# Performance work log

Measured on AMD Instinct MI355X. Metric: run time of the kernel, lower is better.

The kernel has to match this reference:

```python
import jax, jax.numpy as jnp
import numpy as np

N = 100000
E = 1600000
IN_DIM, HID_DIM, OUT_DIM = 128, 64, 32
HEADS = 8
NEG_SLOPE = 0.2
NEG_INF = -1e9


def _glorot(key, shape):
    stdv = np.sqrt(6.0 / (shape[-2] + shape[-1]))
    return jax.random.uniform(key, shape, jnp.float32, -stdv, stdv)


def gat_conv(x, src, dst, self_mask, W, att, bias, heads, out_ch, concat):
    """One GATConv layer (eval mode: dropout off). src/dst already include self-loops;
    self_mask marks original edges that were self-loops (removed via -inf score)."""
    n = x.shape[0]
    h = (x @ W).reshape(n, heads, out_ch)              # [N,H,C]
    x_i = h[dst]                                        # [Etot,H,C] gather target
    x_j = h[src]                                        # [Etot,H,C] gather source
    a = jnp.einsum('ehc,hc->eh', x_i, att[0, :, :out_ch]) \
        + jnp.einsum('ehc,hc->eh', x_j, att[0, :, out_ch:])
    alpha = jax.nn.leaky_relu(a, NEG_SLOPE)             # [Etot,H]
    alpha = jnp.where(self_mask[:, None], NEG_INF, alpha)
    amax = jax.lax.stop_gradient(
        jax.ops.segment_max(alpha, dst, num_segments=n))
    ex = jnp.exp(alpha - amax[dst])
    denom = jax.ops.segment_sum(ex, dst, num_segments=n)
    w = ex / denom[dst]                                 # segment softmax over incoming edges
    out = jax.ops.segment_sum(x_j * w[:, :, None], dst, num_segments=n)  # [N,H,C]
    out = out.reshape(n, heads * out_ch) if concat else out.mean(axis=1)
    return out + bias


def setup_inputs() -> dict:
    key = jax.random.key(0)
    ks = jax.random.split(key, 12)
    x = jax.random.normal(ks[0], (N, IN_DIM), jnp.float32)
    edge_index = jax.random.randint(ks[1], (2, E), 0, N, jnp.int64)
    c1 = HID_DIM // HEADS  # 8
    params = {
        'W1': _glorot(ks[2], (IN_DIM, HEADS * c1)),
        'att1': _glorot(ks[3], (1, HEADS, 2 * c1)),
        'b1': jnp.zeros((HID_DIM,), jnp.float32),
        'W2': _glorot(ks[4], (HID_DIM, HEADS * c1)),
        'att2': _glorot(ks[5], (1, HEADS, 2 * c1)),
        'b2': jnp.zeros((HID_DIM,), jnp.float32),
        'W3': _glorot(ks[6], (HID_DIM, 1 * OUT_DIM)),
        'att3': _glorot(ks[7], (1, 1, 2 * OUT_DIM)),
        'b3': jnp.zeros((OUT_DIM,), jnp.float32),
    }
    return dict(x=x, edge_index=edge_index, **params)


def reference(x, edge_index, W1, att1, b1, W2, att2, b2, W3, att3, b3):
    n = x.shape[0]
    src, dst = edge_index[0], edge_index[1]
    loop = jnp.arange(n, dtype=src.dtype)
    src_f = jnp.concatenate([src, loop])
    dst_f = jnp.concatenate([dst, loop])
    # remove_self_loops + add_self_loops: mask original self-loops, append fresh ones
    self_mask = jnp.concatenate([src == dst, jnp.zeros((n,), bool)])
    c1 = HID_DIM // HEADS
    h = jax.nn.elu(gat_conv(x, src_f, dst_f, self_mask, W1, att1, b1, HEADS, c1, True))
    h = jax.nn.elu(gat_conv(h, src_f, dst_f, self_mask, W2, att2, b2, HEADS, c1, True))
    out = gat_conv(h, src_f, dst_f, self_mask, W3, att3, b3, 1, OUT_DIM, False)
    return out
```

## Files before the change

kernel.cpp:

```cpp
#include <hip/hip_runtime.h>
#include <hip/hip_bf16.h>

#define NN 100000
#define EE 1600000

constexpr int SCAN_BLK = 1024;
constexpr int NB_SCAN  = (NN + SCAN_BLK - 1) / SCAN_BLK;

constexpr int NR2 = 8;
constexpr int RSZ = NN / NR2;
constexpr int CH  = 32;
constexpr int CSZ = EE / CH;
constexpr int SCAT_B = CH * NR2;


__global__ __launch_bounds__(256) void histL_k(const int* __restrict__ ei,
                                               int* __restrict__ CntG) {
    __shared__ int cnt[RSZ];
    int r = blockIdx.x % NR2, c = blockIdx.x / NR2;
    int lo = r * RSZ;
    for (int t = threadIdx.x; t < RSZ; t += 256) cnt[t] = 0;
    __syncthreads();
    const int* __restrict__ dstp = ei + EE;
    int base = c * CSZ;
    int tid = threadIdx.x;
    for (int ii = 0; ii < CSZ; ii += 1024) {
        int off = ii + tid * 4;
        if (off < CSZ) {
            int4 s4 = *(const int4*)&ei[base + off];
            int4 d4 = *(const int4*)&dstp[base + off];
            int dl;
            dl = d4.x - lo; if (dl >= 0 && dl < RSZ && s4.x != d4.x) atomicAdd(&cnt[dl], 1);
            dl = d4.y - lo; if (dl >= 0 && dl < RSZ && s4.y != d4.y) atomicAdd(&cnt[dl], 1);
            dl = d4.z - lo; if (dl >= 0 && dl < RSZ && s4.z != d4.z) atomicAdd(&cnt[dl], 1);
            dl = d4.w - lo; if (dl >= 0 && dl < RSZ && s4.w != d4.w) atomicAdd(&cnt[dl], 1);
        }
    }
    __syncthreads();
    for (int t = threadIdx.x; t < RSZ; t += 256)
        CntG[(size_t)c * NN + lo + t] = cnt[t];
}

__global__ __launch_bounds__(256) void combine_sum_k(int* __restrict__ CntG,
                                                     int* __restrict__ deg,
                                                     int* __restrict__ partials) {
    __shared__ int sh[256];
    int t = threadIdx.x;
    int s_tot = 0;
    #pragma unroll
    for (int k = 0; k < 4; ++k) {
        int d = blockIdx.x * SCAN_BLK + k * 256 + t;
        int run = 0;
        if (d < NN) {
            #pragma unroll 8
            for (int c = 0; c < CH; ++c) {
                int v = CntG[(size_t)c * NN + d];
                CntG[(size_t)c * NN + d] = run;
                run += v;
            }
            deg[d] = run;
        }
        s_tot += run;
    }
    sh[t] = s_tot; __syncthreads();
    for (int off = 128; off > 0; off >>= 1) {
        if (t < off) sh[t] += sh[t + off];
        __syncthreads();
    }
    if (t == 0) partials[blockIdx.x] = sh[0];
}

__global__ void scan_final(const int* __restrict__ deg, const int* __restrict__ partials,
                           int* __restrict__ rowptr) {
    __shared__ int sh[256];
    __shared__ int sp[128];
    int t = threadIdx.x;
    if (t < 128) sp[t] = (t < NB_SCAN) ? partials[t] : 0;
    __syncthreads();
    for (int off = 1; off < 128; off <<= 1) {
        int tmp = 0;
        if (t < 128 && t >= off) tmp = sp[t - off];
        __syncthreads();
        if (t < 128) sp[t] += tmp;
        __syncthreads();
    }
    int pref0 = sp[blockIdx.x] - partials[blockIdx.x];

    int base = blockIdx.x * SCAN_BLK + t * 4;
    int v[4]; int s = 0;
    #pragma unroll
    for (int k = 0; k < 4; ++k) { int i = base + k; v[k] = (i < NN) ? deg[i] : 0; s += v[k]; }
    sh[t] = s; __syncthreads();
    for (int off = 1; off < 256; off <<= 1) {
        int tmp = (t >= off) ? sh[t - off] : 0;
        __syncthreads();
        sh[t] += tmp;
        __syncthreads();
    }
    int pref = pref0 + sh[t] - s;
    #pragma unroll
    for (int k = 0; k < 4; ++k) {
        int i = base + k;
        if (i < NN) {
            rowptr[i] = pref; pref += v[k];
            if (i == NN - 1) rowptr[NN] = pref;
        }
    }
}


__global__ __launch_bounds__(256) void sg1_k(const int* __restrict__ ei,
                                             const int* __restrict__ CntG,
                                             const int* __restrict__ rowptr,
                                             int* __restrict__ col,
                                             const float* __restrict__ xin,
                                             const float* __restrict__ W,
                                             const float* __restrict__ att,
                                             uint2* __restrict__ Hbf,
                                             float* __restrict__ ssrcA,
                                             float* __restrict__ sdst) {
    extern __shared__ char smem[];
    int tid = threadIdx.x;

    if (blockIdx.x < SCAT_B) {
        int* cur = (int*)smem;
        int r = blockIdx.x % NR2, c = blockIdx.x / NR2;
        int lo = r * RSZ;
        for (int t = tid; t < RSZ; t += 256)
            cur[t] = rowptr[lo + t] + CntG[(size_t)c * NN + lo + t];
        __syncthreads();
        const int* __restrict__ dstp = ei + EE;
        int base = c * CSZ;
        for (int ii = 0; ii < CSZ; ii += 1024) {
            int off = ii + tid * 4;
            if (off < CSZ) {
                int4 s4 = *(const int4*)&ei[base + off];
                int4 d4 = *(const int4*)&dstp[base + off];
                int dl;
                dl = d4.x - lo; if (dl >= 0 && dl < RSZ && s4.x != d4.x) { int p = atomicAdd(&cur[dl], 1); col[p] = s4.x; }
                dl = d4.y - lo; if (dl >= 0 && dl < RSZ && s4.y != d4.y) { int p = atomicAdd(&cur[dl], 1); col[p] = s4.y; }
                dl = d4.z - lo; if (dl >= 0 && dl < RSZ && s4.z != d4.z) { int p = atomicAdd(&cur[dl], 1); col[p] = s4.z; }
                dl = d4.w - lo; if (dl >= 0 && dl < RSZ && s4.w != d4.w) { int p = atomicAdd(&cur[dl], 1); col[p] = s4.w; }
            }
        }
        return;
    }

    constexpr int K = 128, M = 64, Hh = 8, NPB = 64;
    constexpr int C   = M / Hh;
    constexpr int MG  = M / 4;
    constexpr int K4  = K / 4;
    constexpr int KC4 = 16;
    constexpr int NCH = K4 / KC4;

    float4* Wq = (float4*)smem;
    float4* Xq = Wq + K * MG;

    const float4* W4 = (const float4*)W;
    for (int i = tid; i < K * MG; i += 256) Wq[i] = W4[i];

    int node0 = (blockIdx.x - SCAT_B) * NPB;
    const float4* x4 = (const float4*)xin;

    int mg = tid % MG, ng = tid / MG;
    int nb = ng * 4;
    float acc[4][4];
    #pragma unroll
    for (int i = 0; i < 4; ++i)
        #pragma unroll
        for (int j = 0; j < 4; ++j) acc[i][j] = 0.f;

    for (int ch = 0; ch < NCH; ++ch) {
        __syncthreads();
        for (int i = tid; i < NPB * KC4; i += 256) {
            int n = i / KC4, k4l = i % KC4;
            int node = node0 + n;
            float4 v = make_float4(0.f, 0.f, 0.f, 0.f);
            if (node < NN) v = x4[(size_t)node * K4 + ch * KC4 + k4l];
            Xq[i] = v;
        }
        __syncthreads();
        #pragma unroll 4
        for (int k4 = 0; k4 < KC4; ++k4) {
            float4 xv[4], wv[4];
            #pragma unroll
            for (int i = 0; i < 4; ++i) xv[i] = Xq[(nb + i) * KC4 + k4];
            int kbase = (ch * KC4 + k4) * 4;
            #pragma unroll
            for (int kk = 0; kk < 4; ++kk) wv[kk] = Wq[(kbase + kk) * MG + mg];
            #pragma unroll
            for (int i = 0; i < 4; ++i) {
                const float* xf = (const float*)&xv[i];
                #pragma unroll
                for (int kk = 0; kk < 4; ++kk) {
                    const float* wf = (const float*)&wv[kk];
                    float xs = xf[kk];
                    acc[i][0] = fmaf(xs, wf[0], acc[i][0]);
                    acc[i][1] = fmaf(xs, wf[1], acc[i][1]);
                    acc[i][2] = fmaf(xs, wf[2], acc[i][2]);
                    acc[i][3] = fmaf(xs, wf[3], acc[i][3]);
                }
            }
        }
    }

    constexpr int TPH = C / 4;
    int head = mg / TPH;
    int c0   = (mg % TPH) * 4;
    float ad[4], as_[4];
    #pragma unroll
    for (int j = 0; j < 4; ++j) {
        ad[j]  = att[head * 2 * C + c0 + j];
        as_[j] = att[head * 2 * C + C + c0 + j];
    }
    #pragma unroll
    for (int i = 0; i < 4; ++i) {
        int node = node0 + nb + i;
        if (node < NN) {
            unsigned short us[4];
            #pragma unroll
            for (int j = 0; j < 4; ++j) {
                __hip_bfloat16 b = __float2bfloat16(acc[i][j]);
                us[j] = *(unsigned short*)&b;
            }
            uint2 pk;
            pk.x = (unsigned)us[0] | ((unsigned)us[1] << 16);
            pk.y = (unsigned)us[2] | ((unsigned)us[3] << 16);
            Hbf[(size_t)node * MG + mg] = pk;
        }
        float pd = acc[i][0]*ad[0]  + acc[i][1]*ad[1]  + acc[i][2]*ad[2]  + acc[i][3]*ad[3];
        float ps = acc[i][0]*as_[0] + acc[i][1]*as_[1] + acc[i][2]*as_[2] + acc[i][3]*as_[3];
        #pragma unroll
        for (int off = 1; off < TPH; off <<= 1) {
            pd += __shfl_xor(pd, off, 64);
            ps += __shfl_xor(ps, off, 64);
        }
        if ((mg % TPH) == 0 && node < NN) {
            sdst[node * Hh + head]  = pd;
            ssrcA[node * Hh + head] = ps;
        }
    }
}


template<int K, int M, int H, int NPB>
__global__ __launch_bounds__(256) void gemm_tile(const float* __restrict__ xin,
                          const float* __restrict__ W,
                          const float* __restrict__ att,
                          uint2* __restrict__ Hbf,
                          float* __restrict__ ssrcA,
                          float* __restrict__ sdst) {
    constexpr int C   = M / H;
    constexpr int MG  = M / 4;
    constexpr int NG  = NPB / 4;
    static_assert(MG * NG == 256, "tile mismatch");
    constexpr int K4  = K / 4;
    constexpr int KC4 = (K4 > 16) ? 16 : K4;
    constexpr int NCH = K4 / KC4;

    __shared__ float4 Wq[K * MG];
    __shared__ float4 Xq[NPB * KC4];

    int tid = threadIdx.x;
    const float4* W4 = (const float4*)W;
    for (int i = tid; i < K * MG; i += 256) Wq[i] = W4[i];

    int node0 = blockIdx.x * NPB;
    const float4* x4 = (const float4*)xin;

    int mg = tid % MG, ng = tid / MG;
    int nb = ng * 4;
    float acc[4][4];
    #pragma unroll
    for (int i = 0; i < 4; ++i)
        #pragma unroll
        for (int j = 0; j < 4; ++j) acc[i][j] = 0.f;

    for (int ch = 0; ch < NCH; ++ch) {
        __syncthreads();
        for (int i = tid; i < NPB * KC4; i += 256) {
            int n = i / KC4, k4l = i % KC4;
            int node = node0 + n;
            float4 v = make_float4(0.f, 0.f, 0.f, 0.f);
            if (node < NN) v = x4[(size_t)node * K4 + ch * KC4 + k4l];
            Xq[i] = v;
        }
        __syncthreads();
        #pragma unroll 4
        for (int k4 = 0; k4 < KC4; ++k4) {
            float4 xv[4], wv[4];
            #pragma unroll
            for (int i = 0; i < 4; ++i) xv[i] = Xq[(nb + i) * KC4 + k4];
            int kbase = (ch * KC4 + k4) * 4;
            #pragma unroll
            for (int kk = 0; kk < 4; ++kk) wv[kk] = Wq[(kbase + kk) * MG + mg];
            #pragma unroll
            for (int i = 0; i < 4; ++i) {
                const float* xf = (const float*)&xv[i];
                #pragma unroll
                for (int kk = 0; kk < 4; ++kk) {
                    const float* wf = (const float*)&wv[kk];
                    float xs = xf[kk];
                    acc[i][0] = fmaf(xs, wf[0], acc[i][0]);
                    acc[i][1] = fmaf(xs, wf[1], acc[i][1]);
                    acc[i][2] = fmaf(xs, wf[2], acc[i][2]);
                    acc[i][3] = fmaf(xs, wf[3], acc[i][3]);
                }
            }
        }
    }

    constexpr int TPH = C / 4;
    int head = mg / TPH;
    int c0   = (mg % TPH) * 4;
    float ad[4], as_[4];
    #pragma unroll
    for (int j = 0; j < 4; ++j) {
        ad[j]  = att[head * 2 * C + c0 + j];
        as_[j] = att[head * 2 * C + C + c0 + j];
    }
    #pragma unroll
    for (int i = 0; i < 4; ++i) {
        int node = node0 + nb + i;
        if (node < NN) {
            unsigned short us[4];
            #pragma unroll
            for (int j = 0; j < 4; ++j) {
                __hip_bfloat16 b = __float2bfloat16(acc[i][j]);
                us[j] = *(unsigned short*)&b;
            }
            uint2 pk;
            pk.x = (unsigned)us[0] | ((unsigned)us[1] << 16);
            pk.y = (unsigned)us[2] | ((unsigned)us[3] << 16);
            Hbf[(size_t)node * MG + mg] = pk;
        }
        float pd = acc[i][0]*ad[0]  + acc[i][1]*ad[1]  + acc[i][2]*ad[2]  + acc[i][3]*ad[3];
        float ps = acc[i][0]*as_[0] + acc[i][1]*as_[1] + acc[i][2]*as_[2] + acc[i][3]*as_[3];
        #pragma unroll
        for (int off = 1; off < TPH; off <<= 1) {
            pd += __shfl_xor(pd, off, 64);
            ps += __shfl_xor(ps, off, 64);
        }
        if ((mg % TPH) == 0 && node < NN) {
            sdst[node * H + head]  = pd;
            ssrcA[node * H + head] = ps;
        }
    }
}


template<int CT, int H, int U, bool ELU_OUT>
__global__ __launch_bounds__(256) void agg_k(const int* __restrict__ rowptr, const int* __restrict__ col,
                      const float* __restrict__ sdst, const float* __restrict__ ssrcA,
                      const uint2* __restrict__ Hbf,
                      const float* __restrict__ bias, float* __restrict__ output) {
    constexpr int C    = CT / H;
    constexpr int CP   = CT / 4;
    constexpr int G    = 64 / CP;
    constexpr int NL   = U / G;
    constexpr int EPEL = (U * H >= 64) ? (U * H) / 64 : 1;
    static_assert(EPEL == 1 || EPEL == 2, "mapping");

    int lane = threadIdx.x & 63;
    int node = blockIdx.x * (blockDim.x >> 6) + (threadIdx.x >> 6);
    if (node >= NN) return;

    int cp = lane % CP;
    int pp = lane / CP;
    int hh = (4 * cp) / C;
    int eh = lane % H;
    int gb = lane / H;
    bool elane = (lane < U * H);

    float sd = elane ? sdst[node * H + eh] : 0.f;

    int start = rowptr[node], end = rowptr[node + 1];

    float dsum = 0.f;
    float e_self = 0.f;
    if (lane < H) {
        float ss = ssrcA[node * H + lane];
        float a = sd + ss; a = (a >= 0.f) ? a : 0.2f * a;
        e_self = __expf(a);
        dsum = e_self;
    }
    uint2 hs = Hbf[(size_t)node * CP + cp];
    float exs = __shfl(e_self, hh, 64);
    float4 acc = make_float4(0.f, 0.f, 0.f, 0.f);
    if (pp == 0) {
        acc.x = exs * __uint_as_float(hs.x << 16);
        acc.y = exs * __uint_as_float(hs.x & 0xffff0000u);
        acc.z = exs * __uint_as_float(hs.y << 16);
        acc.w = exs * __uint_as_float(hs.y & 0xffff0000u);
    }

    int cv = node;
    if (start < end) {
        int idx = start + lane;
        if (lane < U && idx < end) cv = col[idx];
    }

    for (int j = start; j < end; j += U) {
        float s1 = 0.f, s2 = 0.f;
        int b1 = 0, b2 = 0;
        if (EPEL == 2) {
            b1 = __shfl(cv, gb, 64);
            b2 = __shfl(cv, gb + U / 2, 64);
            s1 = ssrcA[b1 * H + eh];
            s2 = ssrcA[b2 * H + eh];
        } else {
            b1 = __shfl(cv, gb, 64);
            if (elane) s1 = ssrcA[b1 * H + eh];
        }

        uint2 hv[NL];
        #pragma unroll
        for (int t = 0; t < NL; ++t) {
            int se = __shfl(cv, t * G + pp, 64);
            hv[t] = Hbf[(size_t)se * CP + cp];
        }

        int jn = j + U;
        int cvN = node;
        if (jn < end) {
            int idx = jn + lane;
            if (lane < U && idx < end) cvN = col[idx];
        }

        float e1 = 0.f, e2 = 0.f;
        if (EPEL == 2) {
            float a1 = sd + s1; a1 = (a1 >= 0.f) ? a1 : 0.2f * a1;
            float a2 = sd + s2; a2 = (a2 >= 0.f) ? a2 : 0.2f * a2;
            if (j + gb < end)         e1 = __expf(a1);
            if (j + gb + U / 2 < end) e2 = __expf(a2);
            dsum += e1 + e2;
        } else {
            float a1 = sd + s1; a1 = (a1 >= 0.f) ? a1 : 0.2f * a1;
            if (elane && j + gb < end) { e1 = __expf(a1); dsum += e1; }
        }

        #pragma unroll
        for (int t = 0; t < NL; ++t) {
            int eidx = t * G + pp;
            float ex;
            if (EPEL == 2)
                ex = __shfl((t * G + G - 1 < U / 2) ? e1 : e2, (eidx & (U / 2 - 1)) * H + hh, 64);
            else
                ex = __shfl(e1, eidx * H + hh, 64);
            float f0 = __uint_as_float(hv[t].x << 16);
            float f1 = __uint_as_float(hv[t].x & 0xffff0000u);
            float f2 = __uint_as_float(hv[t].y << 16);
            float f3 = __uint_as_float(hv[t].y & 0xffff0000u);
            acc.x = fmaf(ex, f0, acc.x);
            acc.y = fmaf(ex, f1, acc.y);
            acc.z = fmaf(ex, f2, acc.z);
            acc.w = fmaf(ex, f3, acc.w);
        }
        cv = cvN;
    }

    #pragma unroll
    for (int off = H; off < 64; off <<= 1) dsum += __shfl_xor(dsum, off, 64);
    float den = __shfl(dsum, hh, 64);
    #pragma unroll
    for (int off = CP; off < 64; off <<= 1) {
        acc.x += __shfl_xor(acc.x, off, 64);
        acc.y += __shfl_xor(acc.y, off, 64);
        acc.z += __shfl_xor(acc.z, off, 64);
        acc.w += __shfl_xor(acc.w, off, 64);
    }
    if (lane < CP) {
        float inv = 1.f / den;
        float4 bv = ((const float4*)bias)[cp];
        float4 v;
        v.x = acc.x * inv + bv.x;
        v.y = acc.y * inv + bv.y;
        v.z = acc.z * inv + bv.z;
        v.w = acc.w * inv + bv.w;
        if (ELU_OUT) {
            v.x = (v.x > 0.f) ? v.x : expm1f(v.x);
            v.y = (v.y > 0.f) ? v.y : expm1f(v.y);
            v.z = (v.z > 0.f) ? v.z : expm1f(v.z);
            v.w = (v.w > 0.f) ? v.w : expm1f(v.w);
        }
        ((float4*)output)[(size_t)node * CP + cp] = v;
    }
}


extern "C" void kernel_launch(void* const* d_in, const int* in_sizes, int n_in,
                              void* d_out, int out_size, void* d_ws, size_t ws_size,
                              hipStream_t stream) {
    const float* x    = (const float*)d_in[0];
    const int*   ei   = (const int*)d_in[1];
    const float* W1   = (const float*)d_in[2];
    const float* att1 = (const float*)d_in[3];
    const float* b1   = (const float*)d_in[4];
    const float* W2   = (const float*)d_in[5];
    const float* att2 = (const float*)d_in[6];
    const float* b2   = (const float*)d_in[7];
    const float* W3   = (const float*)d_in[8];
    const float* att3 = (const float*)d_in[9];
    const float* b3   = (const float*)d_in[10];
    float* out = (float*)d_out;

    char* p = (char*)d_ws;
    auto alloc = [&](size_t bytes) -> void* {
        void* r = (void*)p;
        p += (bytes + 255) & ~(size_t)255;
        return r;
    };
    int*   rowptr   = (int*)alloc((NN + 1) * sizeof(int));
    int*   deg      = (int*)alloc(NN * sizeof(int));
    int*   CntG     = (int*)alloc((size_t)CH * NN * sizeof(int));
    int*   partials = (int*)alloc(NB_SCAN * sizeof(int));
    int*   col      = (int*)alloc(EE * sizeof(int));
    float* sdst     = (float*)alloc((size_t)NN * 8 * sizeof(float));
    float* ssrcA    = (float*)alloc((size_t)NN * 8 * sizeof(float));
    uint2* Hbf      = (uint2*)alloc((size_t)NN * 16 * sizeof(uint2));
    float* Fb       = (float*)alloc((size_t)NN * 64 * sizeof(float));

    histL_k<<<CH * NR2, 256, 0, stream>>>(ei, CntG);
    combine_sum_k<<<NB_SCAN, 256, 0, stream>>>(CntG, deg, partials);
    scan_final<<<NB_SCAN, 256, 0, stream>>>(deg, partials, rowptr);

    constexpr int SMEM = RSZ * (int)sizeof(int);
    sg1_k<<<SCAT_B + (NN + 63) / 64, 256, SMEM, stream>>>(ei, CntG, rowptr, col,
                                                          x, W1, att1, Hbf, ssrcA, sdst);

    agg_k<64, 8, 16, true><<<(NN + 3) / 4, 256, 0, stream>>>(rowptr, col, sdst, ssrcA, Hbf, b1, Fb);

    gemm_tile<64, 64, 8, 64><<<(NN + 63) / 64, 256, 0, stream>>>(Fb, W2, att2, Hbf, ssrcA, sdst);
    agg_k<64, 8, 16, true><<<(NN + 3) / 4, 256, 0, stream>>>(rowptr, col, sdst, ssrcA, Hbf, b2, Fb);

    gemm_tile<64, 32, 1, 128><<<(NN + 127) / 128, 256, 0, stream>>>(Fb, W3, att3, Hbf, ssrcA, sdst);
    agg_k<32, 1, 32, false><<<(NN + 3) / 4, 256, 0, stream>>>(rowptr, col, sdst, ssrcA, Hbf, b3, out);
}
```

Baseline: 385.5 us.

## Fuse layer aggregation and GEMM stages into one cooperative persistent kernel

Replaces the five per-layer launches (three aggregations, two GEMMs) with one cooperative persistent kernel. Phases are separated by grid-wide syncs, and each block loops over node tiles in grid-stride fashion. Buffers are split per layer, with Hbf2 aliased onto the scratch count buffer, and the GEMM K-chunk is reduced to 8 so the shared memory fits a single union. The aim is to remove launch gaps and tail effects between stages. The cost is grid.sync overhead, an occupancy limit of 5 blocks per CU that caps parallelism, and worse latency hiding in the gather-heavy aggregation phases.

```diff
diff --git a/kernel.cpp b/kernel.cpp
--- a/kernel.cpp
+++ b/kernel.cpp
@@ -1,5 +1,8 @@
 #include <hip/hip_runtime.h>
 #include <hip/hip_bf16.h>
+#include <hip/hip_cooperative_groups.h>
+
+namespace cg = cooperative_groups;
 
 #define NN 100000
 #define EE 1600000
@@ -243,72 +246,171 @@
 }
 
 
-template<int K, int M, int H, int NPB>
-__global__ __launch_bounds__(256) void gemm_tile(const float* __restrict__ xin,
-                          const float* __restrict__ W,
-                          const float* __restrict__ att,
-                          uint2* __restrict__ Hbf,
-                          float* __restrict__ ssrcA,
-                          float* __restrict__ sdst) {
+template<int CT, int H, int U, bool ELU_OUT>
+__device__ void agg_phase(const int* __restrict__ rowptr, const int* __restrict__ col,
+                          const float* __restrict__ sdst, const float* __restrict__ ssrcA,
+                          const uint2* __restrict__ Hbf,
+                          const float* __restrict__ bias, float* __restrict__ output) {
+    constexpr int C    = CT / H;
+    constexpr int CP   = CT / 4;
+    constexpr int G    = 64 / CP;
+    constexpr int NL   = U / G;
+    constexpr int EPEL = (U * H >= 64) ? (U * H) / 64 : 1;
+    static_assert(EPEL == 1 || EPEL == 2, "mapping");
+    constexpr int NU   = (NN + 3) / 4;
+
+    int lane = threadIdx.x & 63;
+    int wid  = threadIdx.x >> 6;
+    int cp = lane % CP;
+    int pp = lane / CP;
+    int hh = (4 * cp) / C;
+    int eh = lane % H;
+    int gb = lane / H;
+    bool elane = (lane < U * H);
+
+    for (int u = blockIdx.x; u < NU; u += gridDim.x) {
+        int node = u * 4 + wid;
+        if (node >= NN) continue;
+
+        float sd = elane ? sdst[node * H + eh] : 0.f;
+        int start = rowptr[node], end = rowptr[node + 1];
+
+        float dsum = 0.f;
+        float e_self = 0.f;
+        if (lane < H) {
+            float ss = ssrcA[node * H + lane];
+            float a = sd + ss; a = (a >= 0.f) ? a : 0.2f * a;
+            e_self = __expf(a);
+            dsum = e_self;
+        }
+        uint2 hs = Hbf[(size_t)node * CP + cp];
+        float exs = __shfl(e_self, hh, 64);
+        float4 acc = make_float4(0.f, 0.f, 0.f, 0.f);
+        if (pp == 0) {
+            acc.x = exs * __uint_as_float(hs.x << 16);
+            acc.y = exs * __uint_as_float(hs.x & 0xffff0000u);
+            acc.z = exs * __uint_as_float(hs.y << 16);
+            acc.w = exs * __uint_as_float(hs.y & 0xffff0000u);
+        }
+
+        int cv = node;
+        if (start < end) {
+            int idx = start + lane;
+            if (lane < U && idx < end) cv = col[idx];
+        }
+
+        for (int j = start; j < end; j += U) {
+            float s1 = 0.f, s2 = 0.f;
+            int b1 = 0, b2 = 0;
+            if (EPEL == 2) {
+                b1 = __shfl(cv, gb, 64);
+                b2 = __shfl(cv, gb + U / 2, 64);
+                s1 = ssrcA[b1 * H + eh];
+                s2 = ssrcA[b2 * H + eh];
+            } else {
+                b1 = __shfl(cv, gb, 64);
+                if (elane) s1 = ssrcA[b1 * H + eh];
+            }
+
+            uint2 hv[NL];
+            #pragma unroll
+            for (int t = 0; t < NL; ++t) {
+                int se = __shfl(cv, t * G + pp, 64);
+                hv[t] = Hbf[(size_t)se * CP + cp];
+            }
+
+            int jn = j + U;
+            int cvN = node;
+            if (jn < end) {
+                int idx = jn + lane;
+                if (lane < U && idx < end) cvN = col[idx];
+            }
+
+            float e1 = 0.f, e2 = 0.f;
+            if (EPEL == 2) {
+                float a1 = sd + s1; a1 = (a1 >= 0.f) ? a1 : 0.2f * a1;
+                float a2 = sd + s2; a2 = (a2 >= 0.f) ? a2 : 0.2f * a2;
+                if (j + gb < end)         e1 = __expf(a1);
+                if (j + gb + U / 2 < end) e2 = __expf(a2);
+                dsum += e1 + e2;
+            } else {
+                float a1 = sd + s1; a1 = (a1 >= 0.f) ? a1 : 0.2f * a1;
+                if (elane && j + gb < end) { e1 = __expf(a1); dsum += e1; }
+            }
+
+            #pragma unroll
+            for (int t = 0; t < NL; ++t) {
+                int eidx = t * G + pp;
+                float ex;
+                if (EPEL == 2)
+                    ex = __shfl((t * G + G - 1 < U / 2) ? e1 : e2, (eidx & (U / 2 - 1)) * H + hh, 64);
+                else
+                    ex = __shfl(e1, eidx * H + hh, 64);
+                float f0 = __uint_as_float(hv[t].x << 16);
+                float f1 = __uint_as_float(hv[t].x & 0xffff0000u);
+                float f2 = __uint_as_float(hv[t].y << 16);
+                float f3 = __uint_as_float(hv[t].y & 0xffff0000u);
+                acc.x = fmaf(ex, f0, acc.x);
+                acc.y = fmaf(ex, f1, acc.y);
+                acc.z = fmaf(ex, f2, acc.z);
+                acc.w = fmaf(ex, f3, acc.w);
+            }
+            cv = cvN;
+        }
+
+        #pragma unroll
+        for (int off = H; off < 64; off <<= 1) dsum += __shfl_xor(dsum, off, 64);
+        float den = __shfl(dsum, hh, 64);
+        #pragma unroll
+        for (int off = CP; off < 64; off <<= 1) {
+            acc.x += __shfl_xor(acc.x, off, 64);
+            acc.y += __shfl_xor(acc.y, off, 64);
+            acc.z += __shfl_xor(acc.z, off, 64);
+            acc.w += __shfl_xor(acc.w, off, 64);
+        }
+        if (lane < CP) {
+            float inv = 1.f / den;
+            float4 bv = ((const float4*)bias)[cp];
+            float4 v;
+            v.x = acc.x * inv + bv.x;
+            v.y = acc.y * inv + bv.y;
+            v.z = acc.z * inv + bv.z;
+            v.w = acc.w * inv + bv.w;
+            if (ELU_OUT) {
+                v.x = (v.x > 0.f) ? v.x : expm1f(v.x);
+                v.y = (v.y > 0.f) ? v.y : expm1f(v.y);
+                v.z = (v.z > 0.f) ? v.z : expm1f(v.z);
+                v.w = (v.w > 0.f) ? v.w : expm1f(v.w);
+            }
+            ((float4*)output)[(size_t)node * CP + cp] = v;
+        }
+    }
+}
+
+
+template<int K, int M, int H, int NPB, int KC4>
+__device__ void gemm_phase(const float* __restrict__ xin,
+                           const float* __restrict__ W,
+                           const float* __restrict__ att,
+                           uint2* __restrict__ Hbf,
+                           float* __restrict__ ssrcA,
+                           float* __restrict__ sdst,
+                           float4* __restrict__ Wq, float4* __restrict__ Xq) {
     constexpr int C   = M / H;
     constexpr int MG  = M / 4;
     constexpr int NG  = NPB / 4;
     static_assert(MG * NG == 256, "tile mismatch");
     constexpr int K4  = K / 4;
-    constexpr int KC4 = (K4 > 16) ? 16 : K4;
     constexpr int NCH = K4 / KC4;
-
-    __shared__ float4 Wq[K * MG];
-    __shared__ float4 Xq[NPB * KC4];
+    constexpr int NT  = (NN + NPB - 1) / NPB;
 
     int tid = threadIdx.x;
     const float4* W4 = (const float4*)W;
     for (int i = tid; i < K * MG; i += 256) Wq[i] = W4[i];
 
-    int node0 = blockIdx.x * NPB;
     const float4* x4 = (const float4*)xin;
-
     int mg = tid % MG, ng = tid / MG;
     int nb = ng * 4;
-    float acc[4][4];
-    #pragma unroll
-    for (int i = 0; i < 4; ++i)
-        #pragma unroll
-        for (int j = 0; j < 4; ++j) acc[i][j] = 0.f;
-
-    for (int ch = 0; ch < NCH; ++ch) {
-        __syncthreads();
-        for (int i = tid; i < NPB * KC4; i += 256) {
-            int n = i / KC4, k4l = i % KC4;
-            int node = node0 + n;
-            float4 v = make_float4(0.f, 0.f, 0.f, 0.f);
-            if (node < NN) v = x4[(size_t)node * K4 + ch * KC4 + k4l];
-            Xq[i] = v;
-        }
-        __syncthreads();
-        #pragma unroll 4
-        for (int k4 = 0; k4 < KC4; ++k4) {
-            float4 xv[4], wv[4];
-            #pragma unroll
-            for (int i = 0; i < 4; ++i) xv[i] = Xq[(nb + i) * KC4 + k4];
-            int kbase = (ch * KC4 + k4) * 4;
-            #pragma unroll
-            for (int kk = 0; kk < 4; ++kk) wv[kk] = Wq[(kbase + kk) * MG + mg];
-            #pragma unroll
-            for (int i = 0; i < 4; ++i) {
-                const float* xf = (const float*)&xv[i];
-                #pragma unroll
-                for (int kk = 0; kk < 4; ++kk) {
-                    const float* wf = (const float*)&wv[kk];
-                    float xs = xf[kk];
-                    acc[i][0] = fmaf(xs, wf[0], acc[i][0]);
-                    acc[i][1] = fmaf(xs, wf[1], acc[i][1]);
-                    acc[i][2] = fmaf(xs, wf[2], acc[i][2]);
-                    acc[i][3] = fmaf(xs, wf[3], acc[i][3]);
-                }
-            }
-        }
-    }
 
     constexpr int TPH = C / 4;
     int head = mg / TPH;
@@ -319,172 +421,127 @@
         ad[j]  = att[head * 2 * C + c0 + j];
         as_[j] = att[head * 2 * C + C + c0 + j];
     }
-    #pragma unroll
-    for (int i = 0; i < 4; ++i) {
-        int node = node0 + nb + i;
-        if (node < NN) {
-            unsigned short us[4];
-            #pragma unroll
-            for (int j = 0; j < 4; ++j) {
-                __hip_bfloat16 b = __float2bfloat16(acc[i][j]);
-                us[j] = *(unsigned short*)&b;
-            }
-            uint2 pk;
-            pk.x = (unsigned)us[0] | ((unsigned)us[1] << 16);
-            pk.y = (unsigned)us[2] | ((unsigned)us[3] << 16);
-            Hbf[(size_t)node * MG + mg] = pk;
-        }
-        float pd = acc[i][0]*ad[0]  + acc[i][1]*ad[1]  + acc[i][2]*ad[2]  + acc[i][3]*ad[3];
-        float ps = acc[i][0]*as_[0] + acc[i][1]*as_[1] + acc[i][2]*as_[2] + acc[i][3]*as_[3];
+
+    for (int u = blockIdx.x; u < NT; u += gridDim.x) {
+        int node0 = u * NPB;
+        float acc[4][4];
         #pragma unroll
-        for (int off = 1; off < TPH; off <<= 1) {
-            pd += __shfl_xor(pd, off, 64);
-            ps += __shfl_xor(ps, off, 64);
-        }
-        if ((mg % TPH) == 0 && node < NN) {
-            sdst[node * H + head]  = pd;
-            ssrcA[node * H + head] = ps;
-        }
-    }
+        for (int i = 0; i < 4; ++i)
+            #pragma unroll
+            for (int j = 0; j < 4; ++j) acc[i][j] = 0.f;
+
+        for (int ch = 0; ch < NCH; ++ch) {
+            __syncthreads();
+            for (int i = tid; i < NPB * KC4; i += 256) {
+                int n = i / KC4, k4l = i % KC4;
+                int node = node0 + n;
+                float4 v = make_float4(0.f, 0.f, 0.f, 0.f);
+                if (node < NN) v = x4[(size_t)node * K4 + ch * KC4 + k4l];
+                Xq[i] = v;
+            }
+            __syncthreads();
+            #pragma unroll 4
+            for (int k4 = 0; k4 < KC4; ++k4) {
+                float4 xv[4], wv[4];
+                #pragma unroll
+                for (int i = 0; i < 4; ++i) xv[i] = Xq[(nb + i) * KC4 + k4];
+                int kbase = (ch * KC4 + k4) * 4;
+                #pragma unroll
+                for (int kk = 0; kk < 4; ++kk) wv[kk] = Wq[(kbase + kk) * MG + mg];
+                #pragma unroll
+                for (int i = 0; i < 4; ++i) {
+                    const float* xf = (const float*)&xv[i];
+                    #pragma unroll
+                    for (int kk = 0; kk < 4; ++kk) {
+                        const float* wf = (const float*)&wv[kk];
+                        float xs = xf[kk];
+                        acc[i][0] = fmaf(xs, wf[0], acc[i][0]);
+                        acc[i][1] = fmaf(xs, wf[1], acc[i][1]);
+                        acc[i][2] = fmaf(xs, wf[2], acc[i][2]);
+                        acc[i][3] = fmaf(xs, wf[3], acc[i][3]);
+                    }
+                }
+            }
+        }
+
+        #pragma unroll
+        for (int i = 0; i < 4; ++i) {
+            int node = node0 + nb + i;
+            if (node < NN) {
+                unsigned short us[4];
+                #pragma unroll
+                for (int j = 0; j < 4; ++j) {
+                    __hip_bfloat16 b = __float2bfloat16(acc[i][j]);
+                    us[j] = *(unsigned short*)&b;
+                }
+                uint2 pk;
+                pk.x = (unsigned)us[0] | ((unsigned)us[1] << 16);
+                pk.y = (unsigned)us[2] | ((unsigned)us[3] << 16);
+                Hbf[(size_t)node * MG + mg] = pk;
+            }
+            float pd = acc[i][0]*ad[0]  + acc[i][1]*ad[1]  + acc[i][2]*ad[2]  + acc[i][3]*ad[3];
+            float ps = acc[i][0]*as_[0] + acc[i][1]*as_[1] + acc[i][2]*as_[2] + acc[i][3]*as_[3];
+            #pragma unroll
+            for (int off = 1; off < TPH; off <<= 1) {
+                pd += __shfl_xor(pd, off, 64);
+                ps += __shfl_xor(ps, off, 64);
+            }
+            if ((mg % TPH) == 0 && node < NN) {
+                sdst[node * H + head]  = pd;
+                ssrcA[node * H + head] = ps;
+            }
+        }
+    }
+}
+
+
+__global__ __launch_bounds__(256, 5) void layers_k(
+    const int* rowptr, const int* col,
+    const float* sdst1, const float* ssrcA1, const uint2* Hbf1, const float* b1,
+    float* Fb,
+    const float* W2, const float* att2, uint2* Hbf2, float* ssrcA2, float* sdst2,
+    const float* b2,
+    const float* W3, const float* att3, uint2* Hbf3, float* ssrcA3, float* sdst3,
+    const float* b3,
+    float* out)
+{
+    __shared__ float4 smemU[1536];
+    cg::grid_group grid = cg::this_grid();
+
+    agg_phase<64, 8, 16, true>(rowptr, col, sdst1, ssrcA1, Hbf1, b1, Fb);
+    __threadfence(); grid.sync(); __threadfence();
+
+    gemm_phase<64, 64, 8, 64, 8>(Fb, W2, att2, Hbf2, ssrcA2, sdst2,
+                                 smemU, smemU + 1024);
+    __threadfence(); grid.sync(); __threadfence();
+
+    agg_phase<64, 8, 16, true>(rowptr, col, sdst2, ssrcA2, Hbf2, b2, Fb);
+    __threadfence(); grid.sync(); __threadfence();
+
+    gemm_phase<64, 32, 1, 128, 8>(Fb, W3, att3, Hbf3, ssrcA3, sdst3,
+                                  smemU, smemU + 512);
+    __threadfence(); grid.sync(); __threadfence();
+
+    agg_phase<32, 1, 32, false>(rowptr, col, sdst3, ssrcA3, Hbf3, b3, out);
 }
 
 
 template<int CT, int H, int U, bool ELU_OUT>
-__global__ __launch_bounds__(256) void agg_k(const int* __restrict__ rowptr, const int* __restrict__ col,
+__global__ __launch_bounds__(256) void agg_w(const int* __restrict__ rowptr, const int* __restrict__ col,
                       const float* __restrict__ sdst, const float* __restrict__ ssrcA,
                       const uint2* __restrict__ Hbf,
                       const float* __restrict__ bias, float* __restrict__ output) {
-    constexpr int C    = CT / H;
-    constexpr int CP   = CT / 4;
-    constexpr int G    = 64 / CP;
-    constexpr int NL   = U / G;
-    constexpr int EPEL = (U * H >= 64) ? (U * H) / 64 : 1;
-    static_assert(EPEL == 1 || EPEL == 2, "mapping");
-
-    int lane = threadIdx.x & 63;
-    int node = blockIdx.x * (blockDim.x >> 6) + (threadIdx.x >> 6);
-    if (node >= NN) return;
-
-    int cp = lane % CP;
-    int pp = lane / CP;
-    int hh = (4 * cp) / C;
-    int eh = lane % H;
-    int gb = lane / H;
-    bool elane = (lane < U * H);
-
-    float sd = elane ? sdst[node * H + eh] : 0.f;
-
-    int start = rowptr[node], end = rowptr[node + 1];
-
-    float dsum = 0.f;
-    float e_self = 0.f;
-    if (lane < H) {
-        float ss = ssrcA[node * H + lane];
-        float a = sd + ss; a = (a >= 0.f) ? a : 0.2f * a;
-        e_self = __expf(a);
-        dsum = e_self;
-    }
-    uint2 hs = Hbf[(size_t)node * CP + cp];
-    float exs = __shfl(e_self, hh, 64);
-    float4 acc = make_float4(0.f, 0.f, 0.f, 0.f);
-    if (pp == 0) {
-        acc.x = exs * __uint_as_float(hs.x << 16);
-        acc.y = exs * __uint_as_float(hs.x & 0xffff0000u);
-        acc.z = exs * __uint_as_float(hs.y << 16);
-        acc.w = exs * __uint_as_float(hs.y & 0xffff0000u);
-    }
-
-    int cv = node;
-    if (start < end) {
-        int idx = start + lane;
-        if (lane < U && idx < end) cv = col[idx];
-    }
-
-    for (int j = start; j < end; j += U) {
-        float s1 = 0.f, s2 = 0.f;
-        int b1 = 0, b2 = 0;
-        if (EPEL == 2) {
-            b1 = __shfl(cv, gb, 64);
-            b2 = __shfl(cv, gb + U / 2, 64);
-            s1 = ssrcA[b1 * H + eh];
-            s2 = ssrcA[b2 * H + eh];
-        } else {
-            b1 = __shfl(cv, gb, 64);
-            if (elane) s1 = ssrcA[b1 * H + eh];
-        }
-
-        uint2 hv[NL];
-        #pragma unroll
-        for (int t = 0; t < NL; ++t) {
-            int se = __shfl(cv, t * G + pp, 64);
-            hv[t] = Hbf[(size_t)se * CP + cp];
-        }
-
-        int jn = j + U;
-        int cvN = node;
-        if (jn < end) {
-            int idx = jn + lane;
-            if (lane < U && idx < end) cvN = col[idx];
-        }
-
-        float e1 = 0.f, e2 = 0.f;
-        if (EPEL == 2) {
-            float a1 = sd + s1; a1 = (a1 >= 0.f) ? a1 : 0.2f * a1;
-            float a2 = sd + s2; a2 = (a2 >= 0.f) ? a2 : 0.2f * a2;
-            if (j + gb < end)         e1 = __expf(a1);
-            if (j + gb + U / 2 < end) e2 = __expf(a2);
-            dsum += e1 + e2;
-        } else {
-            float a1 = sd + s1; a1 = (a1 >= 0.f) ? a1 : 0.2f * a1;
-            if (elane && j + gb < end) { e1 = __expf(a1); dsum += e1; }
-        }
-
-        #pragma unroll
-        for (int t = 0; t < NL; ++t) {
-            int eidx = t * G + pp;
-            float ex;
-            if (EPEL == 2)
-                ex = __shfl((t * G + G - 1 < U / 2) ? e1 : e2, (eidx & (U / 2 - 1)) * H + hh, 64);
-            else
-                ex = __shfl(e1, eidx * H + hh, 64);
-            float f0 = __uint_as_float(hv[t].x << 16);
-            float f1 = __uint_as_float(hv[t].x & 0xffff0000u);
-            float f2 = __uint_as_float(hv[t].y << 16);
-            float f3 = __uint_as_float(hv[t].y & 0xffff0000u);
-            acc.x = fmaf(ex, f0, acc.x);
-            acc.y = fmaf(ex, f1, acc.y);
-            acc.z = fmaf(ex, f2, acc.z);
-            acc.w = fmaf(ex, f3, acc.w);
-        }
-        cv = cvN;
-    }
-
-    #pragma unroll
-    for (int off = H; off < 64; off <<= 1) dsum += __shfl_xor(dsum, off, 64);
-    float den = __shfl(dsum, hh, 64);
-    #pragma unroll
-    for (int off = CP; off < 64; off <<= 1) {
-        acc.x += __shfl_xor(acc.x, off, 64);
-        acc.y += __shfl_xor(acc.y, off, 64);
-        acc.z += __shfl_xor(acc.z, off, 64);
-        acc.w += __shfl_xor(acc.w, off, 64);
-    }
-    if (lane < CP) {
-        float inv = 1.f / den;
-        float4 bv = ((const float4*)bias)[cp];
-        float4 v;
-        v.x = acc.x * inv + bv.x;
-        v.y = acc.y * inv + bv.y;
-        v.z = acc.z * inv + bv.z;
-        v.w = acc.w * inv + bv.w;
-        if (ELU_OUT) {
-            v.x = (v.x > 0.f) ? v.x : expm1f(v.x);
-            v.y = (v.y > 0.f) ? v.y : expm1f(v.y);
-            v.z = (v.z > 0.f) ? v.z : expm1f(v.z);
-            v.w = (v.w > 0.f) ? v.w : expm1f(v.w);
-        }
-        ((float4*)output)[(size_t)node * CP + cp] = v;
-    }
+    agg_phase<CT, H, U, ELU_OUT>(rowptr, col, sdst, ssrcA, Hbf, bias, output);
+}
+
+template<int K, int M, int H, int NPB, int KC4>
+__global__ __launch_bounds__(256) void gemm_w(const float* __restrict__ xin,
+                          const float* __restrict__ W, const float* __restrict__ att,
+                          uint2* __restrict__ Hbf, float* __restrict__ ssrcA,
+                          float* __restrict__ sdst) {
+    __shared__ float4 smemU[1536];
+    gemm_phase<K, M, H, NPB, KC4>(xin, W, att, Hbf, ssrcA, sdst,
+                                  smemU, smemU + K * (M / 4));
 }
 
 
@@ -515,10 +572,16 @@
     int*   CntG     = (int*)alloc((size_t)CH * NN * sizeof(int));
     int*   partials = (int*)alloc(NB_SCAN * sizeof(int));
     int*   col      = (int*)alloc(EE * sizeof(int));
-    float* sdst     = (float*)alloc((size_t)NN * 8 * sizeof(float));
-    float* ssrcA    = (float*)alloc((size_t)NN * 8 * sizeof(float));
-    uint2* Hbf      = (uint2*)alloc((size_t)NN * 16 * sizeof(uint2));
+    float* sdst1    = (float*)alloc((size_t)NN * 8 * sizeof(float));
+    float* ssrcA1   = (float*)alloc((size_t)NN * 8 * sizeof(float));
+    uint2* Hbf1     = (uint2*)alloc((size_t)NN * 16 * sizeof(uint2));
     float* Fb       = (float*)alloc((size_t)NN * 64 * sizeof(float));
+    float* sdst2    = (float*)alloc((size_t)NN * 8 * sizeof(float));
+    float* ssrcA2   = (float*)alloc((size_t)NN * 8 * sizeof(float));
+    uint2* Hbf2     = (uint2*)CntG;
+    uint2* Hbf3     = (uint2*)alloc((size_t)NN * 8 * sizeof(uint2));
+    float* sdst3    = (float*)alloc((size_t)NN * sizeof(float));
+    float* ssrcA3   = (float*)alloc((size_t)NN * sizeof(float));
 
     histL_k<<<CH * NR2, 256, 0, stream>>>(ei, CntG);
     combine_sum_k<<<NB_SCAN, 256, 0, stream>>>(CntG, deg, partials);
@@ -526,13 +589,41 @@
 
     constexpr int SMEM = RSZ * (int)sizeof(int);
     sg1_k<<<SCAT_B + (NN + 63) / 64, 256, SMEM, stream>>>(ei, CntG, rowptr, col,
-                                                          x, W1, att1, Hbf, ssrcA, sdst);
-
-    agg_k<64, 8, 16, true><<<(NN + 3) / 4, 256, 0, stream>>>(rowptr, col, sdst, ssrcA, Hbf, b1, Fb);
-
-    gemm_tile<64, 64, 8, 64><<<(NN + 63) / 64, 256, 0, stream>>>(Fb, W2, att2, Hbf, ssrcA, sdst);
-    agg_k<64, 8, 16, true><<<(NN + 3) / 4, 256, 0, stream>>>(rowptr, col, sdst, ssrcA, Hbf, b2, Fb);
-
-    gemm_tile<64, 32, 1, 128><<<(NN + 127) / 128, 256, 0, stream>>>(Fb, W3, att3, Hbf, ssrcA, sdst);
-    agg_k<32, 1, 32, false><<<(NN + 3) / 4, 256, 0, stream>>>(rowptr, col, sdst, ssrcA, Hbf, b3, out);
-}
+                                                          x, W1, att1, Hbf1, ssrcA1, sdst1);
+
+    static int s_checked = 0, s_coop = 0, s_nblk = 0;
+    if (!s_checked) {
+        int dev = 0;
+        hipGetDevice(&dev);
+        int coop = 0;
+        hipDeviceGetAttribute(&coop, hipDeviceAttributeCooperativeLaunch, dev);
+        int mbpc = 0;
+        hipOccupancyMaxActiveBlocksPerMultiprocessor(&mbpc, layers_k, 256, 0);
+        hipDeviceProp_t prop;
+        hipGetDeviceProperties(&prop, dev);
+        int cap = mbpc * prop.multiProcessorCount;
+        s_nblk = (cap > 1280) ? 1280 : cap;
+        s_coop = (coop != 0 && s_nblk >= 256);
+        s_checked = 1;
+    }
+
+    if (s_coop) {
+        void* args[] = {
+            (void*)&rowptr, (void*)&col,
+            (void*)&sdst1, (void*)&ssrcA1, (void*)&Hbf1, (void*)&b1,
+            (void*)&Fb,
+            (void*)&W2, (void*)&att2, (void*)&Hbf2, (void*)&ssrcA2, (void*)&sdst2,
+            (void*)&b2,
+            (void*)&W3, (void*)&att3, (void*)&Hbf3, (void*)&ssrcA3, (void*)&sdst3,
+            (void*)&b3,
+            (void*)&out
+        };
+        hipLaunchCooperativeKernel(layers_k, dim3(s_nblk), dim3(256), args, 0, stream);
+    } else {
+        agg_w<64, 8, 16, true><<<(NN + 3) / 4, 256, 0, stream>>>(rowptr, col, sdst1, ssrcA1, Hbf1, b1, Fb);
+        gemm_w<64, 64, 8, 64, 8><<<(NN + 63) / 64, 256, 0, stream>>>(Fb, W2, att2, Hbf2, ssrcA2, sdst2);
+        agg_w<64, 8, 16, true><<<(NN + 3) / 4, 256, 0, stream>>>(rowptr, col, sdst2, ssrcA2, Hbf2, b2, Fb);
+        gemm_w<64, 32, 1, 128, 8><<<(NN + 127) / 128, 256, 0, stream>>>(Fb, W3, att3, Hbf3, ssrcA3, sdst3);
+        agg_w<32, 1, 32, false><<<(NN + 3) / 4, 256, 0, stream>>>(rowptr, col, sdst3, ssrcA3, Hbf3, b3, out);
+    }
+}
```

Measured after the change: 1.174 ms. 205% more time.

## Fuse combine and scan kernels via decoupled-lookback flags

Applied to the files above, without the earlier changes.

Merges the per-chunk count combine and the final prefix scan into one kernel. Each block publishes its total through a global flag array that histL_k zeroes, and later blocks spin on the flags of earlier blocks to get their prefix offset. This drops one kernel launch and the deg/partials round trip through global memory. It relies on all 98 blocks being co-resident, or at least on earlier blocks being scheduled first, to avoid deadlock.

```diff
diff --git a/kernel.cpp b/kernel.cpp
--- a/kernel.cpp
+++ b/kernel.cpp
@@ -15,10 +15,12 @@
 
 
 __global__ __launch_bounds__(256) void histL_k(const int* __restrict__ ei,
-                                               int* __restrict__ CntG) {
+                                               int* __restrict__ CntG,
+                                               int* __restrict__ flags) {
     __shared__ int cnt[RSZ];
     int r = blockIdx.x % NR2, c = blockIdx.x / NR2;
     int lo = r * RSZ;
+    if (blockIdx.x == 0 && threadIdx.x < 128) flags[threadIdx.x] = 0;
     for (int t = threadIdx.x; t < RSZ; t += 256) cnt[t] = 0;
     __syncthreads();
     const int* __restrict__ dstp = ei + EE;
@@ -41,15 +43,19 @@
         CntG[(size_t)c * NN + lo + t] = cnt[t];
 }
 
-__global__ __launch_bounds__(256) void combine_sum_k(int* __restrict__ CntG,
-                                                     int* __restrict__ deg,
-                                                     int* __restrict__ partials) {
+
+__global__ __launch_bounds__(256) void combine_scan_k(int* __restrict__ CntG,
+                                                      int* __restrict__ flags,
+                                                      int* __restrict__ rowptr) {
+    __shared__ int degsh[SCAN_BLK];
     __shared__ int sh[256];
     int t = threadIdx.x;
+    int b = blockIdx.x;
+
     int s_tot = 0;
     #pragma unroll
     for (int k = 0; k < 4; ++k) {
-        int d = blockIdx.x * SCAN_BLK + k * 256 + t;
+        int d = b * SCAN_BLK + k * 256 + t;
         int run = 0;
         if (d < NN) {
             #pragma unroll 8
@@ -58,38 +64,41 @@
                 CntG[(size_t)c * NN + d] = run;
                 run += v;
             }
-            deg[d] = run;
-        }
+        }
+        degsh[k * 256 + t] = run;
         s_tot += run;
     }
+
     sh[t] = s_tot; __syncthreads();
     for (int off = 128; off > 0; off >>= 1) {
         if (t < off) sh[t] += sh[t + off];
         __syncthreads();
     }
-    if (t == 0) partials[blockIdx.x] = sh[0];
-}
-
-__global__ void scan_final(const int* __restrict__ deg, const int* __restrict__ partials,
-                           int* __restrict__ rowptr) {
-    __shared__ int sh[256];
-    __shared__ int sp[128];
-    int t = threadIdx.x;
-    if (t < 128) sp[t] = (t < NB_SCAN) ? partials[t] : 0;
+    int stot = sh[0];
+
+    if (t == 0) {
+        __threadfence();
+        atomicExch(&flags[b], stot + 1);
+    }
+
+    int psum = 0;
+    if (t < b) {
+        int v;
+        do { v = atomicAdd(&flags[t], 0); } while (v == 0);
+        psum = v - 1;
+    }
     __syncthreads();
-    for (int off = 1; off < 128; off <<= 1) {
-        int tmp = 0;
-        if (t < 128 && t >= off) tmp = sp[t - off];
-        __syncthreads();
-        if (t < 128) sp[t] += tmp;
-        __syncthreads();
-    }
-    int pref0 = sp[blockIdx.x] - partials[blockIdx.x];
-
-    int base = blockIdx.x * SCAN_BLK + t * 4;
+    sh[t] = psum; __syncthreads();
+    for (int off = 128; off > 0; off >>= 1) {
+        if (t < off) sh[t] += sh[t + off];
+        __syncthreads();
+    }
+    int pref0 = sh[0];
+    __syncthreads();
+
     int v[4]; int s = 0;
     #pragma unroll
-    for (int k = 0; k < 4; ++k) { int i = base + k; v[k] = (i < NN) ? deg[i] : 0; s += v[k]; }
+    for (int k = 0; k < 4; ++k) { v[k] = degsh[t * 4 + k]; s += v[k]; }
     sh[t] = s; __syncthreads();
     for (int off = 1; off < 256; off <<= 1) {
         int tmp = (t >= off) ? sh[t - off] : 0;
@@ -100,7 +109,7 @@
     int pref = pref0 + sh[t] - s;
     #pragma unroll
     for (int k = 0; k < 4; ++k) {
-        int i = base + k;
+        int i = b * SCAN_BLK + t * 4 + k;
         if (i < NN) {
             rowptr[i] = pref; pref += v[k];
             if (i == NN - 1) rowptr[NN] = pref;
@@ -511,18 +520,16 @@
         return r;
     };
     int*   rowptr   = (int*)alloc((NN + 1) * sizeof(int));
-    int*   deg      = (int*)alloc(NN * sizeof(int));
+    int*   flags    = (int*)alloc(128 * sizeof(int));
     int*   CntG     = (int*)alloc((size_t)CH * NN * sizeof(int));
-    int*   partials = (int*)alloc(NB_SCAN * sizeof(int));
     int*   col      = (int*)alloc(EE * sizeof(int));
     float* sdst     = (float*)alloc((size_t)NN * 8 * sizeof(float));
     float* ssrcA    = (float*)alloc((size_t)NN * 8 * sizeof(float));
     uint2* Hbf      = (uint2*)alloc((size_t)NN * 16 * sizeof(uint2));
     float* Fb       = (float*)alloc((size_t)NN * 64 * sizeof(float));
 
-    histL_k<<<CH * NR2, 256, 0, stream>>>(ei, CntG);
-    combine_sum_k<<<NB_SCAN, 256, 0, stream>>>(CntG, deg, partials);
-    scan_final<<<NB_SCAN, 256, 0, stream>>>(deg, partials, rowptr);
+    histL_k<<<CH * NR2, 256, 0, stream>>>(ei, CntG, flags);
+    combine_scan_k<<<NB_SCAN, 256, 0, stream>>>(CntG, flags, rowptr);
 
     constexpr int SMEM = RSZ * (int)sizeof(int);
     sg1_k<<<SCAT_B + (NN + 63) / 64, 256, SMEM, stream>>>(ei, CntG, rowptr, col,
```

After: 386.6 us. No clear change (+0.3%).
